# Kernel tuning notes

Measured on AMD Instinct MI355X. Metric: run time of the kernel, lower is better.

The kernel has to match this reference:

```python
import jax, jax.numpy as jnp
import numpy as np

B, S, V, E, H, L = 32, 512, 32000, 256, 512, 48


def setup_inputs() -> dict:
    key = jax.random.key(0)
    ks = jax.random.split(key, 12)
    tokens = jax.random.randint(ks[0], (B, S), 0, V)
    length = jax.random.randint(ks[1], (B,), S // 2, S + 1)
    labels = jax.random.randint(ks[2], (B, S), 0, L)
    embed_table = jax.random.normal(ks[3], (V, E), jnp.float32) * 0.1
    embed_table = embed_table.at[0].set(0.0)  # padding_idx = 0
    # torch LSTM gate order: i, f, g, o ; b = b_ih + b_hh folded together
    w_ih_f = jax.random.normal(ks[4], (4 * H, E), jnp.float32) * 0.05
    w_hh_f = jax.random.normal(ks[5], (4 * H, H), jnp.float32) * 0.05
    b_f = jnp.zeros((4 * H,), jnp.float32)
    w_ih_b = jax.random.normal(ks[6], (4 * H, E), jnp.float32) * 0.05
    w_hh_b = jax.random.normal(ks[7], (4 * H, H), jnp.float32) * 0.05
    b_b = jnp.zeros((4 * H,), jnp.float32)
    w_em = jax.random.normal(ks[8], (L, 2 * H), jnp.float32) * 0.02
    b_em = jnp.zeros((L,), jnp.float32)
    transition = jax.random.uniform(ks[9], (L, L), jnp.float32)  # torch.rand init
    return {"tokens": tokens, "length": length, "labels": labels,
            "embed_table": embed_table,
            "w_ih_f": w_ih_f, "w_hh_f": w_hh_f, "b_f": b_f,
            "w_ih_b": w_ih_b, "w_hh_b": w_hh_b, "b_b": b_b,
            "w_em": w_em, "b_em": b_em, "transition": transition}


def _lstm_dir(x, w_ih, w_hh, b, reverse):
    # x: [B,S,E] -> hidden states [B,S,H]
    xw = jnp.einsum('bse,ge->bsg', x, w_ih) + b  # precompute input projection [B,S,4H]
    if reverse:
        xw = xw[:, ::-1]
    Bn = x.shape[0]
    Hn = w_hh.shape[1]
    h0 = jnp.zeros((Bn, Hn), x.dtype)
    c0 = jnp.zeros((Bn, Hn), x.dtype)

    def step(carry, xt):
        h, c = carry
        gates = xt + h @ w_hh.T  # [B,4H]
        i, f, g, o = jnp.split(gates, 4, axis=-1)
        i = jax.nn.sigmoid(i)
        f = jax.nn.sigmoid(f)
        g = jnp.tanh(g)
        o = jax.nn.sigmoid(o)
        c = f * c + i * g
        h = o * jnp.tanh(c)
        return (h, c), h

    _, hs = jax.lax.scan(step, (h0, c0), jnp.swapaxes(xw, 0, 1))
    hs = jnp.swapaxes(hs, 0, 1)  # [B,S,H]
    if reverse:
        hs = hs[:, ::-1]
    return hs


def reference(tokens, length, labels, embed_table,
              w_ih_f, w_hh_f, b_f, w_ih_b, w_hh_b, b_b,
              w_em, b_em, transition):
    x = embed_table[tokens]                      # [B,S,E]
    hf = _lstm_dir(x, w_ih_f, w_hh_f, b_f, reverse=False)
    hb = _lstm_dir(x, w_ih_b, w_hh_b, b_b, reverse=True)
    h = jnp.concatenate([hf, hb], axis=-1)       # [B,S,2H]
    logits = jnp.einsum('bsh,lh->bsl', h, w_em) + b_em
    e = jnp.exp(logits)                          # emission = exp(linear), as in source
    T = jnp.exp(transition)                      # transition = exp(param), as in source
    Bn, Sn = tokens.shape
    pos = jnp.arange(Sn)[None, :]
    mask = pos < length[:, None]                 # [B,S] valid positions

    # gold path score: sum emissions over valid steps + transitions between them
    em_real = jnp.take_along_axis(e, labels[..., None], axis=-1)[..., 0]  # [B,S]
    real = jnp.sum(em_real * mask, axis=-1)
    trans_real = T[labels[:, :-1], labels[:, 1:]]                          # [B,S-1]
    real = real + jnp.sum(trans_real * mask[:, 1:], axis=-1)

    # forward algorithm, exactly as written in source:
    # alpha_new[k] = logsumexp_l( alpha[k] + T[k,l] + e_t[l] )
    alpha0 = e[:, 0, :]                          # [B,L]

    def step(alpha, inp):
        et, mt = inp                             # [B,L], [B]
        scores = alpha[:, :, None] + T[None, :, :] + et[:, None, :]  # [B,L,L]
        new = jax.nn.logsumexp(scores, axis=-1)
        alpha = jnp.where(mt[:, None], new, alpha)
        return alpha, None

    alpha, _ = jax.lax.scan(step, alpha0,
                            (jnp.swapaxes(e[:, 1:], 0, 1),
                             jnp.swapaxes(mask[:, 1:], 0, 1)))
    sum_score = jax.nn.logsumexp(alpha, axis=-1)  # [B]
    return sum_score - real                       # negative log probability per example
```

## Files before the change

kernel.cpp:

```cpp
#include <hip/hip_runtime.h>
#include <math.h>
#include <stdint.h>

#define Bn 32
#define Sn 512
#define En 256
#define Hn 512
#define Ln 48
#define G4 2048
#define NWG 32
#define SENT16 0x7FFFu

typedef unsigned short u16;
typedef __attribute__((ext_vector_type(8))) __bf16 bf16x8;
typedef __attribute__((ext_vector_type(4))) float f32x4;

__device__ inline float bf2f(u16 u) {
    return __uint_as_float(((unsigned)u) << 16);
}
__device__ inline u16 f2bf(float f) {
    unsigned u = __float_as_uint(f);
    unsigned r = (u + 0x7fffu + ((u >> 16) & 1u)) >> 16;
    return (u16)r;
}
__device__ inline float sigmoidf_(float x) { return 1.f / (1.f + expf(-x)); }
__device__ inline float tanh_fast(float x) { return 2.f / (1.f + expf(-2.f * x)) - 1.f; }

__device__ inline unsigned badMask(f32x4 v) {
    unsigned acc = 0;
    #pragma unroll
    for (int i = 0; i < 4; i++) {
        unsigned d = __float_as_uint(v[i]);
        unsigned x = d ^ 0x7FFF7FFFu;
        acc |= (x - 0x00010001u) & ~x & 0x80008000u;
    }
    return acc;
}

__global__ __launch_bounds__(256) void prep_kernel(
    const int* __restrict__ tokens, const float* __restrict__ embed,
    const float* __restrict__ wihf, const float* __restrict__ wihb,
    const float* __restrict__ whhf, const float* __restrict__ whhb,
    const float* __restrict__ wem, const float* __restrict__ trans,
    u16* __restrict__ xbf, u16* __restrict__ wihf_b, u16* __restrict__ wihb_b,
    u16* __restrict__ whhf_b, u16* __restrict__ whhb_b, u16* __restrict__ wem_b,
    float* __restrict__ expT, float* __restrict__ alphaAcc,
    float* __restrict__ realAcc, unsigned* __restrict__ hf32,
    unsigned* __restrict__ hb32, unsigned* __restrict__ flags)
{
    size_t idx = (size_t)blockIdx.x * blockDim.x + threadIdx.x;
    size_t stride = (size_t)gridDim.x * blockDim.x;
    for (size_t i = idx; i < (size_t)Bn * Sn * En; i += stride) {
        size_t n = i >> 8; int ee = (int)(i & 255);
        int tok = tokens[n];
        xbf[i] = f2bf(embed[(size_t)tok * En + ee]);
    }
    for (size_t i = idx; i < (size_t)G4 * En; i += stride) {
        wihf_b[i] = f2bf(wihf[i]); wihb_b[i] = f2bf(wihb[i]);
    }
    for (size_t i = idx; i < (size_t)G4 * Hn; i += stride) {
        whhf_b[i] = f2bf(whhf[i]); whhb_b[i] = f2bf(whhb[i]);
    }
    for (size_t i = idx; i < (size_t)Ln * 2 * Hn; i += stride) wem_b[i] = f2bf(wem[i]);
    for (size_t i = idx; i < (size_t)Ln * Ln; i += stride) expT[i] = expf(trans[i]);
    for (size_t i = idx; i < (size_t)Bn * Ln; i += stride) alphaAcc[i] = 0.f;
    for (size_t i = idx; i < (size_t)Bn; i += stride) realAcc[i] = 0.f;
    const unsigned sp = (SENT16 << 16) | SENT16;
    for (size_t i = idx; i < (size_t)Bn * Sn * Hn / 2; i += stride) {
        hf32[i] = sp; hb32[i] = sp;
    }
    for (size_t i = idx; i < (size_t)2 * Sn * NWG; i += stride) flags[i] = 0u;
}

__global__ __launch_bounds__(256) void gemm_xw(
    const u16* __restrict__ xbf, const u16* __restrict__ wihf_b,
    const u16* __restrict__ wihb_b, const float* __restrict__ bias_f,
    const float* __restrict__ bias_b, u16* __restrict__ xw_f, u16* __restrict__ xw_b)
{
    int mb = blockIdx.x, nb = blockIdx.y, dir = blockIdx.z;
    const u16* wih = dir ? wihb_b : wihf_b;
    const float* bias = dir ? bias_b : bias_f;
    u16* xw = dir ? xw_b : xw_f;

    __shared__ u16 At[64 * 136];
    __shared__ u16 Bt[64 * 136];

    int tid = threadIdx.x;
    int w = tid >> 6, lane = tid & 63;
    int lm = lane & 15, lkq = (lane >> 4) * 8;
    int Moff = (w & 1) * 32, Noff = (w >> 1) * 32;

    f32x4 zero = {0.f, 0.f, 0.f, 0.f};
    f32x4 acc[2][2] = {{zero, zero}, {zero, zero}};

    for (int kc = 0; kc < 2; kc++) {
        for (int c = tid; c < 1024; c += 256) {
            int r = c >> 4, cc = (c & 15) * 8;
            *(bf16x8*)&At[r * 136 + cc] =
                *(const bf16x8*)&xbf[((size_t)(mb * 64 + r)) * En + kc * 128 + cc];
            *(bf16x8*)&Bt[r * 136 + cc] =
                *(const bf16x8*)&wih[((size_t)(nb * 64 + r)) * En + kc * 128 + cc];
        }
        __syncthreads();
        #pragma unroll
        for (int ks = 0; ks < 4; ks++) {
            int k = ks * 32 + lkq;
            bf16x8 a0 = *(const bf16x8*)&At[(Moff + lm) * 136 + k];
            bf16x8 a1 = *(const bf16x8*)&At[(Moff + 16 + lm) * 136 + k];
            bf16x8 b0 = *(const bf16x8*)&Bt[(Noff + lm) * 136 + k];
            bf16x8 b1 = *(const bf16x8*)&Bt[(Noff + 16 + lm) * 136 + k];
            acc[0][0] = __builtin_amdgcn_mfma_f32_16x16x32_bf16(a0, b0, acc[0][0], 0, 0, 0);
            acc[0][1] = __builtin_amdgcn_mfma_f32_16x16x32_bf16(a0, b1, acc[0][1], 0, 0, 0);
            acc[1][0] = __builtin_amdgcn_mfma_f32_16x16x32_bf16(a1, b0, acc[1][0], 0, 0, 0);
            acc[1][1] = __builtin_amdgcn_mfma_f32_16x16x32_bf16(a1, b1, acc[1][1], 0, 0, 0);
        }
        __syncthreads();
    }
    #pragma unroll
    for (int mi = 0; mi < 2; mi++)
        #pragma unroll
        for (int ni = 0; ni < 2; ni++)
            #pragma unroll
            for (int reg = 0; reg < 4; reg++) {
                int row = Moff + mi * 16 + (lane >> 4) * 4 + reg;
                int col = Noff + ni * 16 + lm;
                int n = mb * 64 + row;
                int g = nb * 64 + col;
                int t = n & 511, b = n >> 9;
                float v = acc[mi][ni][reg] + bias[g];
                xw[((size_t)t * Bn + b) * G4 + g] = f2bf(v);
            }
}

__global__ __launch_bounds__(512) void lstm_rec(
    const u16* __restrict__ whhf_b, const u16* __restrict__ whhb_b,
    const u16* __restrict__ xw_f, const u16* __restrict__ xw_b,
    u16* __restrict__ hf, u16* __restrict__ hb, unsigned* __restrict__ flags)
{
    int wg = blockIdx.x;
    int dir = wg >> 5;
    int w = wg & 31;
    const u16* __restrict__ whh = dir ? whhb_b : whhf_b;
    const u16* __restrict__ xw  = dir ? xw_b  : xw_f;
    u16* __restrict__ hbuf = dir ? hb : hf;
    unsigned* flg = flags + (size_t)dir * Sn * NWG;

    __shared__ u16 Hs[32 * 512];
    __shared__ float Cp[4 * 32 * 17];
    __shared__ u16 hout[32 * 16];

    int tid = threadIdx.x;
    int wv = tid >> 6, lane = tid & 63;
    int lm = lane & 15, kq = lane >> 4;
    int mt = wv & 1, nt = wv >> 1;
    int b = tid >> 4, hc = tid & 15;

    bf16x8 Bf[16];
    {
        const u16* wrow = &whh[((size_t)nt * Hn + (size_t)w * 16 + lm) * Hn];
        #pragma unroll
        for (int ks = 0; ks < 16; ks++)
            Bf[ks] = *(const bf16x8*)&wrow[ks * 32 + kq * 8];
    }

    float c_state = 0.f;
    const f32x4 zero = {0.f, 0.f, 0.f, 0.f};

    for (int it = 0; it < Sn; it++) {
        int t = dir ? (Sn - 1 - it) : it;
        f32x4 acc = zero;

        const u16* xp = &xw[((size_t)t * Bn + b) * G4 + (size_t)w * 16 + hc];
        float xg0 = bf2f(xp[0 * Hn]);
        float xg1 = bf2f(xp[1 * Hn]);
        float xg2 = bf2f(xp[2 * Hn]);
        float xg3 = bf2f(xp[3 * Hn]);

        if (it > 0) {
            int tprev = dir ? (t + 1) : (t - 1);

            if (tid < 64) {
                const unsigned* fp = flg + (size_t)(it - 1) * NWG + (lane & 31);
                int tries = 0;
                while (true) {
                    unsigned v;
                    asm volatile("global_load_dword %0, %1, off sc0 sc1\n\t"
                                 "s_waitcnt vmcnt(0)"
                                 : "=v"(v) : "v"(fp) : "memory");
                    if (__all(v != 0) || ++tries > (1 << 16)) break;
                }
            }
            __syncthreads();

            const u16* base = &hbuf[((size_t)b * Sn + tprev) * Hn];
            const u16* p0 = base + (hc + 0) * 8;
            const u16* p1 = base + (hc + 16) * 8;
            const u16* p2 = base + (hc + 32) * 8;
            const u16* p3 = base + (hc + 48) * 8;
            f32x4 h0, h1, h2, h3;
            int tries = 0;
            while (true) {
                asm volatile(
                    "global_load_dwordx4 %0, %4, off sc0 sc1\n\t"
                    "global_load_dwordx4 %1, %5, off sc0 sc1\n\t"
                    "global_load_dwordx4 %2, %6, off sc0 sc1\n\t"
                    "global_load_dwordx4 %3, %7, off sc0 sc1\n\t"
                    "s_waitcnt vmcnt(0)"
                    : "=v"(h0), "=v"(h1), "=v"(h2), "=v"(h3)
                    : "v"(p0), "v"(p1), "v"(p2), "v"(p3)
                    : "memory");
                if (!(badMask(h0) | badMask(h1) | badMask(h2) | badMask(h3))) break;
                if (++tries > (1 << 16)) break;
            }
            *(f32x4*)&Hs[(b * 64 + ((hc + 0) ^ (b & 7))) * 8] = h0;
            *(f32x4*)&Hs[(b * 64 + ((hc + 16) ^ (b & 7))) * 8] = h1;
            *(f32x4*)&Hs[(b * 64 + ((hc + 32) ^ (b & 7))) * 8] = h2;
            *(f32x4*)&Hs[(b * 64 + ((hc + 48) ^ (b & 7))) * 8] = h3;
            __syncthreads();

            f32x4 aa = zero, ab = zero;
            #pragma unroll
            for (int ks2 = 0; ks2 < 8; ks2++) {
                bf16x8 a0 = *(const bf16x8*)
                    &Hs[((mt * 16 + lm) * 64 + (((2 * ks2) * 4 + kq) ^ (lm & 7))) * 8];
                aa = __builtin_amdgcn_mfma_f32_16x16x32_bf16(a0, Bf[2 * ks2], aa, 0, 0, 0);
                bf16x8 a1 = *(const bf16x8*)
                    &Hs[((mt * 16 + lm) * 64 + (((2 * ks2 + 1) * 4 + kq) ^ (lm & 7))) * 8];
                ab = __builtin_amdgcn_mfma_f32_16x16x32_bf16(a1, Bf[2 * ks2 + 1], ab, 0, 0, 0);
            }
            acc = aa + ab;
        }

        #pragma unroll
        for (int reg = 0; reg < 4; reg++)
            Cp[(nt * 32 + mt * 16 + kq * 4 + reg) * 17 + lm] = acc[reg];
        __syncthreads();

        float g0 = Cp[(0 * 32 + b) * 17 + hc] + xg0;
        float g1 = Cp[(1 * 32 + b) * 17 + hc] + xg1;
        float g2 = Cp[(2 * 32 + b) * 17 + hc] + xg2;
        float g3 = Cp[(3 * 32 + b) * 17 + hc] + xg3;
        float i_ = sigmoidf_(g0);
        float f_ = sigmoidf_(g1);
        float gg = tanh_fast(g2);
        float o_ = sigmoidf_(g3);
        c_state = f_ * c_state + i_ * gg;
        float hv = o_ * tanh_fast(c_state);
        hout[tid] = f2bf(hv);
        __syncthreads();

        if (tid < 64) {
            int bq = lane >> 1, half = lane & 1;
            f32x4 hv8 = *(const f32x4*)&hout[lane * 8];
            u16* sp = &hbuf[((size_t)bq * Sn + t) * Hn + (size_t)w * 16 + half * 8];
            asm volatile("global_store_dwordx4 %0, %1, off sc0 sc1"
                         :: "v"(sp), "v"(hv8) : "memory");
            if (lane == 0) {
                unsigned one = 1;
                unsigned* fq = flg + (size_t)it * NWG + w;
                asm volatile("global_store_dword %0, %1, off sc0 sc1"
                             :: "v"(fq), "v"(one) : "memory");
            }
        }
    }
}

__global__ __launch_bounds__(256) void emis(
    const u16* __restrict__ hf, const u16* __restrict__ hb,
    const u16* __restrict__ wem_b, const float* __restrict__ bem,
    float* __restrict__ e)
{
    int mb = blockIdx.x;
    int tid = threadIdx.x, wv = tid >> 6, lane = tid & 63;
    int lm = lane & 15, lkq = (lane >> 4) * 8;
    int row = mb * 64 + wv * 16;

    f32x4 zero = {0.f, 0.f, 0.f, 0.f};
    f32x4 acc[3] = {zero, zero, zero};
    for (int ks = 0; ks < 32; ks++) {
        int k = ks * 32 + lkq;
        const u16* hsrc = (ks < 16) ? &hf[(size_t)(row + lm) * Hn + k]
                                    : &hb[(size_t)(row + lm) * Hn + (k - 512)];
        bf16x8 a = *(const bf16x8*)hsrc;
        #pragma unroll
        for (int nt = 0; nt < 3; nt++) {
            bf16x8 bfr = *(const bf16x8*)&wem_b[(size_t)(nt * 16 + lm) * 1024 + k];
            acc[nt] = __builtin_amdgcn_mfma_f32_16x16x32_bf16(a, bfr, acc[nt], 0, 0, 0);
        }
    }
    #pragma unroll
    for (int nt = 0; nt < 3; nt++)
        #pragma unroll
        for (int reg = 0; reg < 4; reg++) {
            int r = row + (lane >> 4) * 4 + reg;
            int col = nt * 16 + lm;
            float lg = acc[nt][reg] + bem[col];
            e[(size_t)r * Ln + col] = expf(lg);
        }
}

__global__ __launch_bounds__(64) void crf_step(
    const float* __restrict__ e, const float* __restrict__ expT,
    const int* __restrict__ labels, const int* __restrict__ lengths,
    float* __restrict__ alphaAcc, float* __restrict__ realAcc)
{
    int bt = blockIdx.x;
    int b = bt >> 9, t = bt & 511;
    __shared__ float er[Ln];
    int tid = threadIdx.x;
    if (tid < Ln) er[tid] = e[(size_t)bt * Ln + tid];
    __syncthreads();
    bool inlen = t < lengths[b];
    if (t >= 1 && inlen && tid < Ln) {
        int i = tid;
        float m = -1e30f;
        for (int j = 0; j < Ln; j++) m = fmaxf(m, expT[i * Ln + j] + er[j]);
        float s = 0.f;
        for (int j = 0; j < Ln; j++) s += expf(expT[i * Ln + j] + er[j] - m);
        atomicAdd(&alphaAcc[b * Ln + i], m + logf(s));
    }
    if (tid == 0 && inlen) {
        int lab = labels[b * Sn + t];
        float r = er[lab];
        if (t >= 1) r += expT[labels[b * Sn + t - 1] * Ln + lab];
        atomicAdd(&realAcc[b], r);
    }
}

__global__ __launch_bounds__(64) void finalize(
    const float* __restrict__ e, const float* __restrict__ alphaAcc,
    const float* __restrict__ realAcc, float* __restrict__ out)
{
    int b = threadIdx.x;
    if (b >= Bn) return;
    float m = -1e30f;
    for (int i = 0; i < Ln; i++) {
        float a = e[((size_t)b * Sn) * Ln + i] + alphaAcc[b * Ln + i];
        m = fmaxf(m, a);
    }
    float s = 0.f;
    for (int i = 0; i < Ln; i++) {
        float a = e[((size_t)b * Sn) * Ln + i] + alphaAcc[b * Ln + i];
        s += expf(a - m);
    }
    out[b] = m + logf(s) - realAcc[b];
}

extern "C" void kernel_launch(void* const* d_in, const int* in_sizes, int n_in,
                              void* d_out, int out_size, void* d_ws, size_t ws_size,
                              hipStream_t stream)
{
    const int*   tokens = (const int*)d_in[0];
    const int*   length = (const int*)d_in[1];
    const int*   labels = (const int*)d_in[2];
    const float* embed  = (const float*)d_in[3];
    const float* wihf   = (const float*)d_in[4];
    const float* whhf   = (const float*)d_in[5];
    const float* bf     = (const float*)d_in[6];
    const float* wihb   = (const float*)d_in[7];
    const float* whhb   = (const float*)d_in[8];
    const float* bbv    = (const float*)d_in[9];
    const float* wem    = (const float*)d_in[10];
    const float* bem    = (const float*)d_in[11];
    const float* trans  = (const float*)d_in[12];
    float* out = (float*)d_out;

    char* p = (char*)d_ws;
    auto take = [&](size_t bytes) -> char* {
        char* q = p;
        p += (bytes + 255) & ~(size_t)255;
        return q;
    };
    u16* xw_f   = (u16*)take((size_t)Sn * Bn * G4 * 2);
    u16* xw_b   = (u16*)take((size_t)Sn * Bn * G4 * 2);
    u16* hf     = (u16*)take((size_t)Bn * Sn * Hn * 2);
    u16* hb     = (u16*)take((size_t)Bn * Sn * Hn * 2);
    u16* xbf    = (u16*)take((size_t)Bn * Sn * En * 2);
    u16* wihf_b = (u16*)take((size_t)G4 * En * 2);
    u16* wihb_b = (u16*)take((size_t)G4 * En * 2);
    u16* whhf_b = (u16*)take((size_t)G4 * Hn * 2);
    u16* whhb_b = (u16*)take((size_t)G4 * Hn * 2);
    u16* wem_b  = (u16*)take((size_t)Ln * 2 * Hn * 2);
    float* e        = (float*)take((size_t)Bn * Sn * Ln * 4);
    float* expT     = (float*)take((size_t)Ln * Ln * 4);
    float* alphaAcc = (float*)take((size_t)Bn * Ln * 4);
    float* realAcc  = (float*)take((size_t)Bn * 4);
    unsigned* flags = (unsigned*)take((size_t)2 * Sn * NWG * 4);
    if ((size_t)(p - (char*)d_ws) > ws_size) return;

    prep_kernel<<<4096, 256, 0, stream>>>(tokens, embed, wihf, wihb, whhf, whhb, wem, trans,
                                          xbf, wihf_b, wihb_b, whhf_b, whhb_b, wem_b,
                                          expT, alphaAcc, realAcc,
                                          (unsigned*)hf, (unsigned*)hb, flags);

    dim3 g1(256, 32, 2);
    gemm_xw<<<g1, 256, 0, stream>>>(xbf, wihf_b, wihb_b, bf, bbv, xw_f, xw_b);

    void* ra[] = { (void*)&whhf_b, (void*)&whhb_b, (void*)&xw_f, (void*)&xw_b,
                   (void*)&hf, (void*)&hb, (void*)&flags };
    hipLaunchCooperativeKernel((const void*)lstm_rec, dim3(2 * NWG), dim3(512), ra, 0, stream);

    emis<<<256, 256, 0, stream>>>(hf, hb, wem_b, bem, e);
    crf_step<<<Bn * Sn, 64, 0, stream>>>(e, expT, labels, length, alphaAcc, realAcc);
    finalize<<<1, 64, 0, stream>>>(e, alphaAcc, realAcc, out);
}
```

Before: 1.987 ms.

## Interleave forward and backward LSTM directions in one workgroup, drop flag polling

The recurrent kernel now runs 32 workgroups instead of 64, and each one processes both directions in alternating phases, holding both W_hh slices in registers. The per-step flag array and its polling are removed. Readiness of h is now detected only by polling the sentinel-initialised h buffer. The intent is that one direction's global-memory latency overlaps the other direction's work, and that the extra flag round trip goes away. In exchange, register pressure doubles for the weight fragments, half as many CUs are used, and each workgroup's serial chain gets longer.

```diff
diff --git a/kernel.cpp b/kernel.cpp
--- a/kernel.cpp
+++ b/kernel.cpp
@@ -46,7 +46,7 @@
     u16* __restrict__ whhf_b, u16* __restrict__ whhb_b, u16* __restrict__ wem_b,
     float* __restrict__ expT, float* __restrict__ alphaAcc,
     float* __restrict__ realAcc, unsigned* __restrict__ hf32,
-    unsigned* __restrict__ hb32, unsigned* __restrict__ flags)
+    unsigned* __restrict__ hb32)
 {
     size_t idx = (size_t)blockIdx.x * blockDim.x + threadIdx.x;
     size_t stride = (size_t)gridDim.x * blockDim.x;
@@ -69,7 +69,6 @@
     for (size_t i = idx; i < (size_t)Bn * Sn * Hn / 2; i += stride) {
         hf32[i] = sp; hb32[i] = sp;
     }
-    for (size_t i = idx; i < (size_t)2 * Sn * NWG; i += stride) flags[i] = 0u;
 }
 
 __global__ __launch_bounds__(256) void gemm_xw(
@@ -132,18 +131,12 @@
             }
 }
 
-__global__ __launch_bounds__(512) void lstm_rec(
+__global__ __launch_bounds__(512, 2) void lstm_rec(
     const u16* __restrict__ whhf_b, const u16* __restrict__ whhb_b,
     const u16* __restrict__ xw_f, const u16* __restrict__ xw_b,
-    u16* __restrict__ hf, u16* __restrict__ hb, unsigned* __restrict__ flags)
-{
-    int wg = blockIdx.x;
-    int dir = wg >> 5;
-    int w = wg & 31;
-    const u16* __restrict__ whh = dir ? whhb_b : whhf_b;
-    const u16* __restrict__ xw  = dir ? xw_b  : xw_f;
-    u16* __restrict__ hbuf = dir ? hb : hf;
-    unsigned* flg = flags + (size_t)dir * Sn * NWG;
+    u16* __restrict__ hf, u16* __restrict__ hb)
+{
+    int w = blockIdx.x;
 
     __shared__ u16 Hs[32 * 512];
     __shared__ float Cp[4 * 32 * 17];
@@ -155,111 +148,100 @@
     int mt = wv & 1, nt = wv >> 1;
     int b = tid >> 4, hc = tid & 15;
 
-    bf16x8 Bf[16];
+    bf16x8 Bf[2][16];
     {
-        const u16* wrow = &whh[((size_t)nt * Hn + (size_t)w * 16 + lm) * Hn];
-        #pragma unroll
-        for (int ks = 0; ks < 16; ks++)
-            Bf[ks] = *(const bf16x8*)&wrow[ks * 32 + kq * 8];
-    }
-
-    float c_state = 0.f;
+        const u16* wrow_f = &whhf_b[((size_t)nt * Hn + (size_t)w * 16 + lm) * Hn];
+        const u16* wrow_b = &whhb_b[((size_t)nt * Hn + (size_t)w * 16 + lm) * Hn];
+        #pragma unroll
+        for (int ks = 0; ks < 16; ks++) {
+            Bf[0][ks] = *(const bf16x8*)&wrow_f[ks * 32 + kq * 8];
+            Bf[1][ks] = *(const bf16x8*)&wrow_b[ks * 32 + kq * 8];
+        }
+    }
+
+    float cs[2] = {0.f, 0.f};
     const f32x4 zero = {0.f, 0.f, 0.f, 0.f};
 
     for (int it = 0; it < Sn; it++) {
-        int t = dir ? (Sn - 1 - it) : it;
-        f32x4 acc = zero;
-
-        const u16* xp = &xw[((size_t)t * Bn + b) * G4 + (size_t)w * 16 + hc];
-        float xg0 = bf2f(xp[0 * Hn]);
-        float xg1 = bf2f(xp[1 * Hn]);
-        float xg2 = bf2f(xp[2 * Hn]);
-        float xg3 = bf2f(xp[3 * Hn]);
-
-        if (it > 0) {
-            int tprev = dir ? (t + 1) : (t - 1);
-
-            if (tid < 64) {
-                const unsigned* fp = flg + (size_t)(it - 1) * NWG + (lane & 31);
+        #pragma unroll
+        for (int ph = 0; ph < 2; ph++) {
+            const int dir = ph;
+            int t = dir ? (Sn - 1 - it) : it;
+            const u16* __restrict__ xw = dir ? xw_b : xw_f;
+            u16* __restrict__ hbuf = dir ? hb : hf;
+
+            const u16* xp = &xw[((size_t)t * Bn + b) * G4 + (size_t)w * 16 + hc];
+            float xg0 = bf2f(xp[0 * Hn]);
+            float xg1 = bf2f(xp[1 * Hn]);
+            float xg2 = bf2f(xp[2 * Hn]);
+            float xg3 = bf2f(xp[3 * Hn]);
+
+            f32x4 acc = zero;
+            if (it > 0) {
+                int tprev = dir ? (t + 1) : (t - 1);
+                const u16* base = &hbuf[((size_t)b * Sn + tprev) * Hn];
+                const u16* p0 = base + (hc + 0) * 8;
+                const u16* p1 = base + (hc + 16) * 8;
+                const u16* p2 = base + (hc + 32) * 8;
+                const u16* p3 = base + (hc + 48) * 8;
+                f32x4 h0, h1, h2, h3;
                 int tries = 0;
                 while (true) {
-                    unsigned v;
-                    asm volatile("global_load_dword %0, %1, off sc0 sc1\n\t"
-                                 "s_waitcnt vmcnt(0)"
-                                 : "=v"(v) : "v"(fp) : "memory");
-                    if (__all(v != 0) || ++tries > (1 << 16)) break;
+                    asm volatile(
+                        "global_load_dwordx4 %0, %4, off sc0 sc1\n\t"
+                        "global_load_dwordx4 %1, %5, off sc0 sc1\n\t"
+                        "global_load_dwordx4 %2, %6, off sc0 sc1\n\t"
+                        "global_load_dwordx4 %3, %7, off sc0 sc1\n\t"
+                        "s_waitcnt vmcnt(0)"
+                        : "=v"(h0), "=v"(h1), "=v"(h2), "=v"(h3)
+                        : "v"(p0), "v"(p1), "v"(p2), "v"(p3)
+                        : "memory");
+                    if (!(badMask(h0) | badMask(h1) | badMask(h2) | badMask(h3))) break;
+                    if (++tries > (1 << 16)) break;
                 }
+                *(f32x4*)&Hs[(b * 64 + ((hc + 0) ^ (b & 7))) * 8] = h0;
+                *(f32x4*)&Hs[(b * 64 + ((hc + 16) ^ (b & 7))) * 8] = h1;
+                *(f32x4*)&Hs[(b * 64 + ((hc + 32) ^ (b & 7))) * 8] = h2;
+                *(f32x4*)&Hs[(b * 64 + ((hc + 48) ^ (b & 7))) * 8] = h3;
+                __syncthreads();
+
+                f32x4 aa = zero, ab = zero;
+                #pragma unroll
+                for (int ks2 = 0; ks2 < 8; ks2++) {
+                    bf16x8 a0 = *(const bf16x8*)
+                        &Hs[((mt * 16 + lm) * 64 + (((2 * ks2) * 4 + kq) ^ (lm & 7))) * 8];
+                    aa = __builtin_amdgcn_mfma_f32_16x16x32_bf16(a0, Bf[dir][2 * ks2], aa, 0, 0, 0);
+                    bf16x8 a1 = *(const bf16x8*)
+                        &Hs[((mt * 16 + lm) * 64 + (((2 * ks2 + 1) * 4 + kq) ^ (lm & 7))) * 8];
+                    ab = __builtin_amdgcn_mfma_f32_16x16x32_bf16(a1, Bf[dir][2 * ks2 + 1], ab, 0, 0, 0);
+                }
+                acc = aa + ab;
             }
+
+            #pragma unroll
+            for (int reg = 0; reg < 4; reg++)
+                Cp[(nt * 32 + mt * 16 + kq * 4 + reg) * 17 + lm] = acc[reg];
             __syncthreads();
 
-            const u16* base = &hbuf[((size_t)b * Sn + tprev) * Hn];
-            const u16* p0 = base + (hc + 0) * 8;
-            const u16* p1 = base + (hc + 16) * 8;
-            const u16* p2 = base + (hc + 32) * 8;
-            const u16* p3 = base + (hc + 48) * 8;
-            f32x4 h0, h1, h2, h3;
-            int tries = 0;
-            while (true) {
-                asm volatile(
-                    "global_load_dwordx4 %0, %4, off sc0 sc1\n\t"
-                    "global_load_dwordx4 %1, %5, off sc0 sc1\n\t"
-                    "global_load_dwordx4 %2, %6, off sc0 sc1\n\t"
-                    "global_load_dwordx4 %3, %7, off sc0 sc1\n\t"
-                    "s_waitcnt vmcnt(0)"
-                    : "=v"(h0), "=v"(h1), "=v"(h2), "=v"(h3)
-                    : "v"(p0), "v"(p1), "v"(p2), "v"(p3)
-                    : "memory");
-                if (!(badMask(h0) | badMask(h1) | badMask(h2) | badMask(h3))) break;
-                if (++tries > (1 << 16)) break;
-            }
-            *(f32x4*)&Hs[(b * 64 + ((hc + 0) ^ (b & 7))) * 8] = h0;
-            *(f32x4*)&Hs[(b * 64 + ((hc + 16) ^ (b & 7))) * 8] = h1;
-            *(f32x4*)&Hs[(b * 64 + ((hc + 32) ^ (b & 7))) * 8] = h2;
-            *(f32x4*)&Hs[(b * 64 + ((hc + 48) ^ (b & 7))) * 8] = h3;
+            float g0 = Cp[(0 * 32 + b) * 17 + hc] + xg0;
+            float g1 = Cp[(1 * 32 + b) * 17 + hc] + xg1;
+            float g2 = Cp[(2 * 32 + b) * 17 + hc] + xg2;
+            float g3 = Cp[(3 * 32 + b) * 17 + hc] + xg3;
+            float i_ = sigmoidf_(g0);
+            float f_ = sigmoidf_(g1);
+            float gg = tanh_fast(g2);
+            float o_ = sigmoidf_(g3);
+            cs[ph] = f_ * cs[ph] + i_ * gg;
+            float hv = o_ * tanh_fast(cs[ph]);
+            hout[tid] = f2bf(hv);
             __syncthreads();
 
-            f32x4 aa = zero, ab = zero;
-            #pragma unroll
-            for (int ks2 = 0; ks2 < 8; ks2++) {
-                bf16x8 a0 = *(const bf16x8*)
-                    &Hs[((mt * 16 + lm) * 64 + (((2 * ks2) * 4 + kq) ^ (lm & 7))) * 8];
-                aa = __builtin_amdgcn_mfma_f32_16x16x32_bf16(a0, Bf[2 * ks2], aa, 0, 0, 0);
-                bf16x8 a1 = *(const bf16x8*)
-                    &Hs[((mt * 16 + lm) * 64 + (((2 * ks2 + 1) * 4 + kq) ^ (lm & 7))) * 8];
-                ab = __builtin_amdgcn_mfma_f32_16x16x32_bf16(a1, Bf[2 * ks2 + 1], ab, 0, 0, 0);
-            }
-            acc = aa + ab;
-        }
-
-        #pragma unroll
-        for (int reg = 0; reg < 4; reg++)
-            Cp[(nt * 32 + mt * 16 + kq * 4 + reg) * 17 + lm] = acc[reg];
-        __syncthreads();
-
-        float g0 = Cp[(0 * 32 + b) * 17 + hc] + xg0;
-        float g1 = Cp[(1 * 32 + b) * 17 + hc] + xg1;
-        float g2 = Cp[(2 * 32 + b) * 17 + hc] + xg2;
-        float g3 = Cp[(3 * 32 + b) * 17 + hc] + xg3;
-        float i_ = sigmoidf_(g0);
-        float f_ = sigmoidf_(g1);
-        float gg = tanh_fast(g2);
-        float o_ = sigmoidf_(g3);
-        c_state = f_ * c_state + i_ * gg;
-        float hv = o_ * tanh_fast(c_state);
-        hout[tid] = f2bf(hv);
-        __syncthreads();
-
-        if (tid < 64) {
-            int bq = lane >> 1, half = lane & 1;
-            f32x4 hv8 = *(const f32x4*)&hout[lane * 8];
-            u16* sp = &hbuf[((size_t)bq * Sn + t) * Hn + (size_t)w * 16 + half * 8];
-            asm volatile("global_store_dwordx4 %0, %1, off sc0 sc1"
-                         :: "v"(sp), "v"(hv8) : "memory");
-            if (lane == 0) {
-                unsigned one = 1;
-                unsigned* fq = flg + (size_t)it * NWG + w;
-                asm volatile("global_store_dword %0, %1, off sc0 sc1"
-                             :: "v"(fq), "v"(one) : "memory");
+            if (tid < 64) {
+                int bq = lane >> 1, half = lane & 1;
+                f32x4 hv8 = *(const f32x4*)&hout[lane * 8];
+                u16* sp = &hbuf[((size_t)bq * Sn + t) * Hn + (size_t)w * 16 + half * 8];
+                asm volatile("global_store_dwordx4 %0, %1, off sc0 sc1"
+                             :: "v"(sp), "v"(hv8) : "memory");
             }
         }
     }
@@ -385,20 +367,19 @@
     float* expT     = (float*)take((size_t)Ln * Ln * 4);
     float* alphaAcc = (float*)take((size_t)Bn * Ln * 4);
     float* realAcc  = (float*)take((size_t)Bn * 4);
-    unsigned* flags = (unsigned*)take((size_t)2 * Sn * NWG * 4);
     if ((size_t)(p - (char*)d_ws) > ws_size) return;
 
     prep_kernel<<<4096, 256, 0, stream>>>(tokens, embed, wihf, wihb, whhf, whhb, wem, trans,
                                           xbf, wihf_b, wihb_b, whhf_b, whhb_b, wem_b,
                                           expT, alphaAcc, realAcc,
-                                          (unsigned*)hf, (unsigned*)hb, flags);
+                                          (unsigned*)hf, (unsigned*)hb);
 
     dim3 g1(256, 32, 2);
     gemm_xw<<<g1, 256, 0, stream>>>(xbf, wihf_b, wihb_b, bf, bbv, xw_f, xw_b);
 
     void* ra[] = { (void*)&whhf_b, (void*)&whhb_b, (void*)&xw_f, (void*)&xw_b,
-                   (void*)&hf, (void*)&hb, (void*)&flags };
-    hipLaunchCooperativeKernel((const void*)lstm_rec, dim3(2 * NWG), dim3(512), ra, 0, stream);
+                   (void*)&hf, (void*)&hb };
+    hipLaunchCooperativeKernel((const void*)lstm_rec, dim3(NWG), dim3(512), ra, 0, stream);
 
     emis<<<256, 256, 0, stream>>>(hf, hb, wem_b, bem, e);
     crf_step<<<Bn * Sn, 64, 0, stream>>>(e, expT, labels, length, alphaAcc, realAcc);
```

New measurement: 2.718 ms. 1.37x slower.
